# Kernel optimization log

Hardware: AMD Instinct MI355X
Metric: run time of the kernel (lower is better)

Reference implementation:

```python
import jax, jax.numpy as jnp
import numpy as np
from jax import lax

T, B, S, D, V = 128, 512, 128, 128, 50257


def setup_inputs() -> dict:
    key = jax.random.key(0)
    ks = jax.random.split(key, 6)
    words = jax.random.randint(ks[0], (T, B), 0, V, dtype=jnp.int64)
    masks = jnp.ones((T, B), dtype=jnp.float32)
    tparams = jax.random.normal(ks[1], (S, S), dtype=jnp.float32)
    tag_embed = jax.random.normal(ks[2], (S, D), dtype=jnp.float32)
    word_embed = jax.random.normal(ks[3], (V, D), dtype=jnp.float32)
    transform = jax.random.normal(ks[4], (D, D), dtype=jnp.float32) * 0.05 + jnp.eye(D, dtype=jnp.float32)
    correction = jax.random.normal(ks[5], (S, V), dtype=jnp.float32) * 0.05
    return {"words": words, "masks": masks, "tparams": tparams,
            "tag_embed": tag_embed, "word_embed": word_embed,
            "transform": transform, "correction": correction}


def reference(words, masks, tparams, tag_embed, word_embed, transform, correction):
    num_state = tparams.shape[0]
    # update_emission (unsupervised mode): project word embeddings, score against tags,
    # add correction, log_softmax over the vocab dimension (dim=0 of (V,S)).
    word_emb = word_embed @ transform                      # (V, D)
    log_emission = jax.nn.log_softmax(word_emb @ tag_embed.T + correction.T, axis=0)  # (V, S)
    # _calc_logA: log-normalized transition matrix (rows = source state)
    logA = jax.nn.log_softmax(tparams, axis=1)             # (S, S)
    # uniform log prior pi = log(1/S)
    log_pi = jnp.full((num_state,), jnp.log(1.0 / num_state), dtype=log_emission.dtype)

    em = log_emission[words]                               # (T, B, S) gathered densities

    alpha0 = log_pi[None, :] + em[0]                       # (B, S)

    def step(alpha, inp):
        dens, m = inp                                      # (B,S), (B,)
        # _forward_cell: logsumexp over previous state of alpha + logA + density
        new = jax.nn.logsumexp(alpha[:, :, None] + logA[None, :, :] + dens[:, None, :], axis=1)
        m = m[:, None]
        alpha = m * new + (1.0 - m) * alpha
        return alpha, None

    alpha, _ = lax.scan(step, alpha0, (em[1:], masks[1:]))
    objective = jnp.sum(jax.nn.logsumexp(alpha, axis=1))
    return -objective
```

## Files before the change

### kernel.cpp

```cpp
#include <hip/hip_runtime.h>
#include <math.h>

#define T_ 128
#define B_ 512
#define S_ 128
#define D_ 128
#define V_ 50257

#define K2_VT 64
#define K2_NB ((V_ + K2_VT - 1) / K2_VT)

__global__ __launch_bounds__(128) void k1_m2(const float* __restrict__ transform,
                                             const float* __restrict__ tag_embed,
                                             float* __restrict__ M2) {
  __shared__ float te[128][129];
  int tid = threadIdx.x;
  for (int r = 0; r < 128; ++r) te[r][tid] = tag_embed[r * 128 + tid];
  __syncthreads();
  int k = blockIdx.x;
  float acc = 0.f;
  #pragma unroll 8
  for (int d = 0; d < 128; ++d) acc += transform[k * 128 + d] * te[tid][d];
  M2[k * 128 + tid] = acc;
}

__global__ __launch_bounds__(64) void k1b_a(const float* __restrict__ tparams,
                                            float* __restrict__ A) {
  int i = blockIdx.x;
  int l = threadIdx.x;
  float x0 = tparams[i * 128 + l];
  float x1 = tparams[i * 128 + 64 + l];
  float m = fmaxf(x0, x1);
  #pragma unroll
  for (int off = 32; off; off >>= 1) m = fmaxf(m, __shfl_xor(m, off));
  float e0 = __expf(x0 - m), e1 = __expf(x1 - m);
  float s = e0 + e1;
  #pragma unroll
  for (int off = 32; off; off >>= 1) s += __shfl_xor(s, off);
  float inv = 1.f / s;
  A[i * 128 + l]      = e0 * inv;
  A[i * 128 + 64 + l] = e1 * inv;
}

__global__ __launch_bounds__(256, 2) void k2_logits(const float* __restrict__ we,
                                                 const float* __restrict__ M2,
                                                 const float* __restrict__ corr,
                                                 float* __restrict__ logits,
                                                 float* __restrict__ pmaxb,
                                                 float* __restrict__ psumb) {
  int tid = threadIdx.x;
  int sc = tid & 31;
  int vg = tid >> 5;
  long v0 = (long)blockIdx.x * K2_VT;
  __shared__ float weT[128][68];
  __shared__ float m2t[64][128];

  #pragma unroll
  for (int it = 0; it < 32; ++it) {
    int idx = it * 256 + tid;
    int d = idx & 127;
    int vv = idx >> 7;
    long v = v0 + vv;
    weT[d][vv] = (v < V_) ? we[v * 128 + d] : 0.f;
  }

  float acc[8][4];
  #pragma unroll
  for (int u = 0; u < 8; ++u)
    #pragma unroll
    for (int e = 0; e < 4; ++e) acc[u][e] = 0.f;

  #pragma unroll
  for (int c = 0; c < 2; ++c) {
    __syncthreads();
    #pragma unroll
    for (int it = 0; it < 32; ++it) {
      int idx = it * 256 + tid;
      int kr = idx >> 7, s = idx & 127;
      m2t[kr][s] = M2[(c * 64 + kr) * 128 + s];
    }
    __syncthreads();
    #pragma unroll 8
    for (int k = 0; k < 64; ++k) {
      float4 mv = *(const float4*)&m2t[k][4 * sc];
      float4 w0 = *(const float4*)&weT[c * 64 + k][8 * vg];
      float4 w1 = *(const float4*)&weT[c * 64 + k][8 * vg + 4];
      acc[0][0] += w0.x * mv.x; acc[0][1] += w0.x * mv.y; acc[0][2] += w0.x * mv.z; acc[0][3] += w0.x * mv.w;
      acc[1][0] += w0.y * mv.x; acc[1][1] += w0.y * mv.y; acc[1][2] += w0.y * mv.z; acc[1][3] += w0.y * mv.w;
      acc[2][0] += w0.z * mv.x; acc[2][1] += w0.z * mv.y; acc[2][2] += w0.z * mv.z; acc[2][3] += w0.z * mv.w;
      acc[3][0] += w0.w * mv.x; acc[3][1] += w0.w * mv.y; acc[3][2] += w0.w * mv.z; acc[3][3] += w0.w * mv.w;
      acc[4][0] += w1.x * mv.x; acc[4][1] += w1.x * mv.y; acc[4][2] += w1.x * mv.z; acc[4][3] += w1.x * mv.w;
      acc[5][0] += w1.y * mv.x; acc[5][1] += w1.y * mv.y; acc[5][2] += w1.y * mv.z; acc[5][3] += w1.y * mv.w;
      acc[6][0] += w1.z * mv.x; acc[6][1] += w1.z * mv.y; acc[6][2] += w1.z * mv.z; acc[6][3] += w1.z * mv.w;
      acc[7][0] += w1.w * mv.x; acc[7][1] += w1.w * mv.y; acc[7][2] += w1.w * mv.z; acc[7][3] += w1.w * mv.w;
    }
  }

  float lm[4], ls[4], Lst[8][4];
  #pragma unroll
  for (int e = 0; e < 4; ++e) { lm[e] = -INFINITY; ls[e] = 0.f; }
  long vbase = v0 + 8 * vg;
  #pragma unroll
  for (int e = 0; e < 4; ++e) {
    long rbase = (long)(4 * sc + e) * V_ + vbase;
    #pragma unroll
    for (int u = 0; u < 8; ++u) {
      if (vbase + u < V_) {
        float L = acc[u][e] + corr[rbase + u];
        Lst[u][e] = L;
        float nm = fmaxf(lm[e], L);
        ls[e] = ls[e] * __expf(lm[e] - nm) + __expf(L - nm);
        lm[e] = nm;
      }
    }
  }
  #pragma unroll
  for (int u = 0; u < 8; ++u) {
    long v = vbase + u;
    if (v < V_) {
      float4 st = make_float4(Lst[u][0], Lst[u][1], Lst[u][2], Lst[u][3]);
      *(float4*)&logits[v * 128 + 4 * sc] = st;
    }
  }

  __syncthreads();
  float* pmx = (float*)m2t;
  float* psm = pmx + 8 * 128;
  #pragma unroll
  for (int e = 0; e < 4; ++e) {
    pmx[vg * 128 + 4 * sc + e] = lm[e];
    psm[vg * 128 + 4 * sc + e] = ls[e];
  }
  __syncthreads();
  if (tid < 128) {
    int s = tid;
    float m = -INFINITY, sum = 0.f;
    #pragma unroll
    for (int g = 0; g < 8; ++g) {
      float pm = pmx[g * 128 + s];
      if (pm > -1e30f) {
        float ps = psm[g * 128 + s];
        float nm = fmaxf(m, pm);
        sum = sum * __expf(m - nm) + ps * __expf(pm - nm);
        m = nm;
      }
    }
    pmaxb[blockIdx.x * 128 + s] = m;
    psumb[blockIdx.x * 128 + s] = sum;
  }
}

__global__ __launch_bounds__(256) void k3_c(const float* __restrict__ pmaxb,
                                            const float* __restrict__ psumb,
                                            float* __restrict__ C) {
  int s = blockIdx.x;
  int t = threadIdx.x;
  float m = -INFINITY, sum = 0.f;
  #pragma unroll
  for (int q = 0; q < 4; ++q) {
    int b = t + q * 256;
    if (b < K2_NB) {
      float pm = pmaxb[b * 128 + s];
      if (pm > -1e30f) {
        float ps = psumb[b * 128 + s];
        float nm = fmaxf(m, pm);
        sum = sum * __expf(m - nm) + ps * __expf(pm - nm);
        m = nm;
      }
    }
  }
  #pragma unroll
  for (int off = 32; off; off >>= 1) {
    float om = __shfl_xor(m, off);
    float os = __shfl_xor(sum, off);
    float nm = fmaxf(m, om);
    sum = sum * __expf(m - nm) + os * __expf(om - nm);
    m = nm;
  }
  __shared__ float wm[4], wsv[4];
  int lane = t & 63, wv = t >> 6;
  if (lane == 0) { wm[wv] = m; wsv[wv] = sum; }
  __syncthreads();
  if (t == 0) {
    float M = fmaxf(fmaxf(wm[0], wm[1]), fmaxf(wm[2], wm[3]));
    float S = wsv[0] * __expf(wm[0] - M) + wsv[1] * __expf(wm[1] - M)
            + wsv[2] * __expf(wm[2] - M) + wsv[3] * __expf(wm[3] - M);
    C[s] = M + __logf(S);
  }
}

__global__ __launch_bounds__(512, 4) void k4_rec(const int* __restrict__ words,
                                              const float* __restrict__ masks,
                                              const float* __restrict__ A,
                                              const float* __restrict__ C,
                                              const float* __restrict__ logits,
                                              float* __restrict__ bv) {
  const float kB = 70.70101247f;
  int tid = threadIdx.x;
  int j = tid & 127;
  int h = tid >> 7;
  int b = blockIdx.x;
  int lane = tid & 63, w = tid >> 6;
  __shared__ __align__(16) float els[128];
  __shared__ float part[4][128];
  __shared__ __align__(16) float pmax4[4];
  __shared__ float wred[2];
  __shared__ int   wbuf[128];
  __shared__ float mbuf[128];
  __shared__ float em[127 * 128];
  if (tid < 128) {
    wbuf[j] = words[j * B_ + b];
    mbuf[j] = masks[j * B_ + b];
  }
  float Ac[32];
  #pragma unroll
  for (int k = 0; k < 32; ++k) Ac[k] = A[(h * 32 + k) * 128 + j];
  float Cj = C[j];
  __syncthreads();

  #pragma unroll 4
  for (int tt = 0; tt < 32; ++tt) {
    int t = tt * 4 + h;
    if (t >= 1) {
      float L = logits[(unsigned)(wbuf[t] * 128 + j)];
      em[(t - 1) * 128 + j] = __expf(L - Cj + kB);
    }
  }

  float a = 0.f, S = 0.f, a0 = 0.f;
  if (tid < 128) {
    a0 = -4.852030263919617f + logits[(unsigned)(wbuf[0] * 128 + j)] - Cj;
    float wm = a0;
    #pragma unroll
    for (int off = 32; off; off >>= 1) wm = fmaxf(wm, __shfl_xor(wm, off));
    if (lane == 0) wred[w] = wm;
  }
  __syncthreads();
  if (tid < 128) {
    float M0 = fmaxf(wred[0], wred[1]);
    a = __expf(a0 - M0);
    S = M0;
    els[j] = a;
  }
  __syncthreads();

  for (int t = 1; t < T_; ++t) {
    float4 e0 = ((const float4*)els)[h * 8 + 0];
    float4 e1 = ((const float4*)els)[h * 8 + 1];
    float4 e2 = ((const float4*)els)[h * 8 + 2];
    float4 e3 = ((const float4*)els)[h * 8 + 3];
    float4 e4 = ((const float4*)els)[h * 8 + 4];
    float4 e5 = ((const float4*)els)[h * 8 + 5];
    float4 e6 = ((const float4*)els)[h * 8 + 6];
    float4 e7 = ((const float4*)els)[h * 8 + 7];
    float p0 = e0.x * Ac[0]  + e0.y * Ac[1]  + e0.z * Ac[2]  + e0.w * Ac[3]
             + e1.x * Ac[4]  + e1.y * Ac[5]  + e1.z * Ac[6]  + e1.w * Ac[7];
    float p1 = e2.x * Ac[8]  + e2.y * Ac[9]  + e2.z * Ac[10] + e2.w * Ac[11]
             + e3.x * Ac[12] + e3.y * Ac[13] + e3.z * Ac[14] + e3.w * Ac[15];
    float p2 = e4.x * Ac[16] + e4.y * Ac[17] + e4.z * Ac[18] + e4.w * Ac[19]
             + e5.x * Ac[20] + e5.y * Ac[21] + e5.z * Ac[22] + e5.w * Ac[23];
    float p3 = e6.x * Ac[24] + e6.y * Ac[25] + e6.z * Ac[26] + e6.w * Ac[27]
             + e7.x * Ac[28] + e7.y * Ac[29] + e7.z * Ac[30] + e7.w * Ac[31];
    part[h][j] = (p0 + p1) + (p2 + p3);
    if (j == 0) {
      float4 ma = make_float4(fmaxf(e0.x, e1.x), fmaxf(e0.y, e1.y), fmaxf(e0.z, e1.z), fmaxf(e0.w, e1.w));
      float4 mb = make_float4(fmaxf(e2.x, e3.x), fmaxf(e2.y, e3.y), fmaxf(e2.z, e3.z), fmaxf(e2.w, e3.w));
      float4 mc = make_float4(fmaxf(e4.x, e5.x), fmaxf(e4.y, e5.y), fmaxf(e4.z, e5.z), fmaxf(e4.w, e5.w));
      float4 md = make_float4(fmaxf(e6.x, e7.x), fmaxf(e6.y, e7.y), fmaxf(e6.z, e7.z), fmaxf(e6.w, e7.w));
      float4 m1 = make_float4(fmaxf(ma.x, mb.x), fmaxf(ma.y, mb.y), fmaxf(ma.z, mb.z), fmaxf(ma.w, mb.w));
      float4 m2 = make_float4(fmaxf(mc.x, md.x), fmaxf(mc.y, md.y), fmaxf(mc.z, md.z), fmaxf(mc.w, md.w));
      float mx = fmaxf(fmaxf(fmaxf(m1.x, m1.y), fmaxf(m1.z, m1.w)),
                       fmaxf(fmaxf(m2.x, m2.y), fmaxf(m2.z, m2.w)));
      pmax4[h] = mx;
    }
    float emv = 0.f, mm = 0.f;
    if (tid < 128) {
      emv = em[(t - 1) * 128 + j];
      mm = mbuf[t];
    }
    __syncthreads();
    if (tid < 128) {
      float4 pm4 = *(const float4*)pmax4;
      float Mst = fmaxf(fmaxf(pm4.x, pm4.y), fmaxf(pm4.z, pm4.w));
      float invM = 1.f / Mst;
      float P = (part[0][j] + part[1][j]) + (part[2][j] + part[3][j]);
      float nv   = (P * invM) * emv;
      float oldq = (a * invM) * 0x1p102f;
      a = mm * nv + (1.f - mm) * oldq;
      els[j] = a;
      S += __logf(Mst) - kB;
    }
    __syncthreads();
  }

  if (tid < 128) {
    float ss = a;
    #pragma unroll
    for (int off = 32; off; off >>= 1) ss += __shfl_xor(ss, off);
    if (lane == 0) wred[w] = ss;
  }
  __syncthreads();
  if (tid == 0) bv[b] = S + __logf(wred[0] + wred[1]);
}

__global__ __launch_bounds__(256) void k5_sum(const float* __restrict__ bv,
                                              float* __restrict__ out) {
  int t = threadIdx.x;
  float s = bv[t] + bv[t + 256];
  #pragma unroll
  for (int off = 32; off; off >>= 1) s += __shfl_xor(s, off);
  __shared__ float wsm[4];
  if ((t & 63) == 0) wsm[t >> 6] = s;
  __syncthreads();
  if (t == 0) out[0] = -(wsm[0] + wsm[1] + wsm[2] + wsm[3]);
}

extern "C" void kernel_launch(void* const* d_in, const int* in_sizes, int n_in,
                              void* d_out, int out_size, void* d_ws, size_t ws_size,
                              hipStream_t stream) {
  const int*   words      = (const int*)d_in[0];
  const float* masks      = (const float*)d_in[1];
  const float* tparams    = (const float*)d_in[2];
  const float* tag_embed  = (const float*)d_in[3];
  const float* word_embed = (const float*)d_in[4];
  const float* transform  = (const float*)d_in[5];
  const float* correction = (const float*)d_in[6];

  float* ws     = (float*)d_ws;
  float* M2     = ws;
  float* A      = ws + 16384;
  float* C      = ws + 32768;
  float* bv     = ws + 32896;
  float* pmaxb  = ws + 33408;
  float* psumb  = ws + 134016;
  float* logits = ws + 234624;

  hipLaunchKernelGGL(k1_m2,    dim3(128),    dim3(128), 0, stream, transform, tag_embed, M2);
  hipLaunchKernelGGL(k1b_a,    dim3(128),    dim3(64),  0, stream, tparams, A);
  hipLaunchKernelGGL(k2_logits,dim3(K2_NB),  dim3(256), 0, stream, word_embed, M2, correction, logits, pmaxb, psumb);
  hipLaunchKernelGGL(k3_c,     dim3(S_),     dim3(256), 0, stream, pmaxb, psumb, C);
  hipLaunchKernelGGL(k4_rec,   dim3(512),    dim3(512), 0, stream, words, masks, A, C, logits, bv);
  hipLaunchKernelGGL(k5_sum,   dim3(1),      dim3(256), 0, stream, bv, (float*)d_out);
}
```

Measured before the change: 194.8 us.

## Restructure forward recursion to one thread per state with double-buffered alpha

```diff
diff --git a/kernel.cpp b/kernel.cpp
--- a/kernel.cpp
+++ b/kernel.cpp
@@ -189,118 +189,121 @@
   }
 }
 
-__global__ __launch_bounds__(512, 4) void k4_rec(const int* __restrict__ words,
-                                              const float* __restrict__ masks,
-                                              const float* __restrict__ A,
-                                              const float* __restrict__ C,
-                                              const float* __restrict__ logits,
-                                              float* __restrict__ bv) {
+#define K4CHAIN8(XA, XB, BASE) \
+  (XA.x * Ac[(BASE)]   + XA.y * Ac[(BASE)+1] + XA.z * Ac[(BASE)+2] + XA.w * Ac[(BASE)+3] + \
+   XB.x * Ac[(BASE)+4] + XB.y * Ac[(BASE)+5] + XB.z * Ac[(BASE)+6] + XB.w * Ac[(BASE)+7])
+
+__global__ __launch_bounds__(128, 1) void k4_rec(const int* __restrict__ words,
+                                                 const float* __restrict__ masks,
+                                                 const float* __restrict__ A,
+                                                 const float* __restrict__ C,
+                                                 const float* __restrict__ logits,
+                                                 float* __restrict__ bv) {
   const float kB = 70.70101247f;
-  int tid = threadIdx.x;
-  int j = tid & 127;
-  int h = tid >> 7;
+  int j = threadIdx.x;
   int b = blockIdx.x;
-  int lane = tid & 63, w = tid >> 6;
-  __shared__ __align__(16) float els[128];
-  __shared__ float part[4][128];
-  __shared__ __align__(16) float pmax4[4];
-  __shared__ float wred[2];
+  int lane = j & 63, w = j >> 6;
+  __shared__ __align__(16) float els[2][128];
+  __shared__ float wmax[2][2];
+  __shared__ float sred[2];
   __shared__ int   wbuf[128];
   __shared__ float mbuf[128];
   __shared__ float em[127 * 128];
-  if (tid < 128) {
-    wbuf[j] = words[j * B_ + b];
-    mbuf[j] = masks[j * B_ + b];
-  }
-  float Ac[32];
-  #pragma unroll
-  for (int k = 0; k < 32; ++k) Ac[k] = A[(h * 32 + k) * 128 + j];
+
+  wbuf[j] = words[j * B_ + b];
+  mbuf[j] = masks[j * B_ + b];
+
+  float Ac[128];
+  #pragma unroll
+  for (int i = 0; i < 128; ++i) Ac[i] = A[i * 128 + j];
   float Cj = C[j];
   __syncthreads();
 
   #pragma unroll 4
-  for (int tt = 0; tt < 32; ++tt) {
-    int t = tt * 4 + h;
-    if (t >= 1) {
-      float L = logits[(unsigned)(wbuf[t] * 128 + j)];
-      em[(t - 1) * 128 + j] = __expf(L - Cj + kB);
-    }
-  }
-
-  float a = 0.f, S = 0.f, a0 = 0.f;
-  if (tid < 128) {
-    a0 = -4.852030263919617f + logits[(unsigned)(wbuf[0] * 128 + j)] - Cj;
-    float wm = a0;
-    #pragma unroll
-    for (int off = 32; off; off >>= 1) wm = fmaxf(wm, __shfl_xor(wm, off));
-    if (lane == 0) wred[w] = wm;
-  }
-  __syncthreads();
-  if (tid < 128) {
-    float M0 = fmaxf(wred[0], wred[1]);
-    a = __expf(a0 - M0);
-    S = M0;
-    els[j] = a;
-  }
+  for (int tt = 0; tt < 127; ++tt) {
+    float L = logits[(unsigned)(wbuf[tt + 1] * 128 + j)];
+    em[tt * 128 + j] = __expf(L - Cj + kB);
+  }
+
+  float a0i = -4.852030263919617f + logits[(unsigned)(wbuf[0] * 128 + j)] - Cj;
+  float wm = a0i;
+  #pragma unroll
+  for (int off = 32; off; off >>= 1) wm = fmaxf(wm, __shfl_xor(wm, off));
+  if (lane == 0) sred[w] = wm;
+  __syncthreads();
+  float M0 = fmaxf(sred[0], sred[1]);
+  float a = __expf(a0i - M0);
+  float S = M0;
+  els[0][j] = a;
+  float wx = a;
+  #pragma unroll
+  for (int off = 32; off; off >>= 1) wx = fmaxf(wx, __shfl_xor(wx, off));
+  if (lane == 0) wmax[0][w] = wx;
   __syncthreads();
 
   for (int t = 1; t < T_; ++t) {
-    float4 e0 = ((const float4*)els)[h * 8 + 0];
-    float4 e1 = ((const float4*)els)[h * 8 + 1];
-    float4 e2 = ((const float4*)els)[h * 8 + 2];
-    float4 e3 = ((const float4*)els)[h * 8 + 3];
-    float4 e4 = ((const float4*)els)[h * 8 + 4];
-    float4 e5 = ((const float4*)els)[h * 8 + 5];
-    float4 e6 = ((const float4*)els)[h * 8 + 6];
-    float4 e7 = ((const float4*)els)[h * 8 + 7];
-    float p0 = e0.x * Ac[0]  + e0.y * Ac[1]  + e0.z * Ac[2]  + e0.w * Ac[3]
-             + e1.x * Ac[4]  + e1.y * Ac[5]  + e1.z * Ac[6]  + e1.w * Ac[7];
-    float p1 = e2.x * Ac[8]  + e2.y * Ac[9]  + e2.z * Ac[10] + e2.w * Ac[11]
-             + e3.x * Ac[12] + e3.y * Ac[13] + e3.z * Ac[14] + e3.w * Ac[15];
-    float p2 = e4.x * Ac[16] + e4.y * Ac[17] + e4.z * Ac[18] + e4.w * Ac[19]
-             + e5.x * Ac[20] + e5.y * Ac[21] + e5.z * Ac[22] + e5.w * Ac[23];
-    float p3 = e6.x * Ac[24] + e6.y * Ac[25] + e6.z * Ac[26] + e6.w * Ac[27]
-             + e7.x * Ac[28] + e7.y * Ac[29] + e7.z * Ac[30] + e7.w * Ac[31];
-    part[h][j] = (p0 + p1) + (p2 + p3);
-    if (j == 0) {
-      float4 ma = make_float4(fmaxf(e0.x, e1.x), fmaxf(e0.y, e1.y), fmaxf(e0.z, e1.z), fmaxf(e0.w, e1.w));
-      float4 mb = make_float4(fmaxf(e2.x, e3.x), fmaxf(e2.y, e3.y), fmaxf(e2.z, e3.z), fmaxf(e2.w, e3.w));
-      float4 mc = make_float4(fmaxf(e4.x, e5.x), fmaxf(e4.y, e5.y), fmaxf(e4.z, e5.z), fmaxf(e4.w, e5.w));
-      float4 md = make_float4(fmaxf(e6.x, e7.x), fmaxf(e6.y, e7.y), fmaxf(e6.z, e7.z), fmaxf(e6.w, e7.w));
-      float4 m1 = make_float4(fmaxf(ma.x, mb.x), fmaxf(ma.y, mb.y), fmaxf(ma.z, mb.z), fmaxf(ma.w, mb.w));
-      float4 m2 = make_float4(fmaxf(mc.x, md.x), fmaxf(mc.y, md.y), fmaxf(mc.z, md.z), fmaxf(mc.w, md.w));
-      float mx = fmaxf(fmaxf(fmaxf(m1.x, m1.y), fmaxf(m1.z, m1.w)),
-                       fmaxf(fmaxf(m2.x, m2.y), fmaxf(m2.z, m2.w)));
-      pmax4[h] = mx;
-    }
-    float emv = 0.f, mm = 0.f;
-    if (tid < 128) {
-      emv = em[(t - 1) * 128 + j];
-      mm = mbuf[t];
-    }
+    const float4* E4 = (const float4*)els[(t + 1) & 1];
+    float G0, G1, G2, G3;
+    {
+      float4 x0 = E4[0], x1 = E4[1], x2 = E4[2], x3 = E4[3];
+      float4 x4 = E4[4], x5 = E4[5], x6 = E4[6], x7 = E4[7];
+      float p0 = K4CHAIN8(x0, x1, 0);
+      float p1 = K4CHAIN8(x2, x3, 8);
+      float p2 = K4CHAIN8(x4, x5, 16);
+      float p3 = K4CHAIN8(x6, x7, 24);
+      G0 = (p0 + p1) + (p2 + p3);
+    }
+    {
+      float4 x0 = E4[8], x1 = E4[9], x2 = E4[10], x3 = E4[11];
+      float4 x4 = E4[12], x5 = E4[13], x6 = E4[14], x7 = E4[15];
+      float p0 = K4CHAIN8(x0, x1, 32);
+      float p1 = K4CHAIN8(x2, x3, 40);
+      float p2 = K4CHAIN8(x4, x5, 48);
+      float p3 = K4CHAIN8(x6, x7, 56);
+      G1 = (p0 + p1) + (p2 + p3);
+    }
+    {
+      float4 x0 = E4[16], x1 = E4[17], x2 = E4[18], x3 = E4[19];
+      float4 x4 = E4[20], x5 = E4[21], x6 = E4[22], x7 = E4[23];
+      float p0 = K4CHAIN8(x0, x1, 64);
+      float p1 = K4CHAIN8(x2, x3, 72);
+      float p2 = K4CHAIN8(x4, x5, 80);
+      float p3 = K4CHAIN8(x6, x7, 88);
+      G2 = (p0 + p1) + (p2 + p3);
+    }
+    {
+      float4 x0 = E4[24], x1 = E4[25], x2 = E4[26], x3 = E4[27];
+      float4 x4 = E4[28], x5 = E4[29], x6 = E4[30], x7 = E4[31];
+      float p0 = K4CHAIN8(x0, x1, 96);
+      float p1 = K4CHAIN8(x2, x3, 104);
+      float p2 = K4CHAIN8(x4, x5, 112);
+      float p3 = K4CHAIN8(x6, x7, 120);
+      G3 = (p0 + p1) + (p2 + p3);
+    }
+    float P = (G0 + G1) + (G2 + G3);
+
+    float Mst = fmaxf(wmax[(t + 1) & 1][0], wmax[(t + 1) & 1][1]);
+    float invM = 1.f / Mst;
+    float emv = em[(t - 1) * 128 + j];
+    float mm = mbuf[t];
+    float nv   = (P * invM) * emv;
+    float oldq = (a * invM) * 0x1p102f;
+    a = mm * nv + (1.f - mm) * oldq;
+    els[t & 1][j] = a;
+    S += __logf(Mst) - kB;
+    float wxx = a;
+    #pragma unroll
+    for (int off = 32; off; off >>= 1) wxx = fmaxf(wxx, __shfl_xor(wxx, off));
+    if (lane == 0) wmax[t & 1][w] = wxx;
     __syncthreads();
-    if (tid < 128) {
-      float4 pm4 = *(const float4*)pmax4;
-      float Mst = fmaxf(fmaxf(pm4.x, pm4.y), fmaxf(pm4.z, pm4.w));
-      float invM = 1.f / Mst;
-      float P = (part[0][j] + part[1][j]) + (part[2][j] + part[3][j]);
-      float nv   = (P * invM) * emv;
-      float oldq = (a * invM) * 0x1p102f;
-      a = mm * nv + (1.f - mm) * oldq;
-      els[j] = a;
-      S += __logf(Mst) - kB;
-    }
-    __syncthreads();
-  }
-
-  if (tid < 128) {
-    float ss = a;
-    #pragma unroll
-    for (int off = 32; off; off >>= 1) ss += __shfl_xor(ss, off);
-    if (lane == 0) wred[w] = ss;
-  }
-  __syncthreads();
-  if (tid == 0) bv[b] = S + __logf(wred[0] + wred[1]);
+  }
+
+  float ss = a;
+  #pragma unroll
+  for (int off = 32; off; off >>= 1) ss += __shfl_xor(ss, off);
+  if (lane == 0) sred[w] = ss;
+  __syncthreads();
+  if (j == 0) bv[b] = S + __logf(sred[0] + sred[1]);
 }
 
 __global__ __launch_bounds__(256) void k5_sum(const float* __restrict__ bv,
@@ -339,6 +342,6 @@
   hipLaunchKernelGGL(k1b_a,    dim3(128),    dim3(64),  0, stream, tparams, A);
   hipLaunchKernelGGL(k2_logits,dim3(K2_NB),  dim3(256), 0, stream, word_embed, M2, correction, logits, pmaxb, psumb);
   hipLaunchKernelGGL(k3_c,     dim3(S_),     dim3(256), 0, stream, pmaxb, psumb, C);
-  hipLaunchKernelGGL(k4_rec,   dim3(512),    dim3(512), 0, stream, words, masks, A, C, logits, bv);
+  hipLaunchKernelGGL(k4_rec,   dim3(512),    dim3(128), 0, stream, words, masks, A, C, logits, bv);
   hipLaunchKernelGGL(k5_sum,   dim3(1),      dim3(256), 0, stream, bv, (float*)d_out);
 }
```

After: 218.3 us. 1.12x slower.
